# Kernel tuning notes

Measured on AMD Instinct MI355X. Metric: run time of the kernel, lower is better.

Reference implementation:

```python
import jax, jax.numpy as jnp
import numpy as np

T = 4096          # total packed tokens
SEG = 512         # segment length (position_ids reset every SEG)
D = 768           # hidden_size
H = 12            # num_attention_heads
DH = D // H       # head_dim = 64
THETA = 160000.0  # global_rope_theta (layer_id=0 -> global attention)


def setup_inputs() -> dict:
    key = jax.random.key(0)
    k1, k2, k3 = jax.random.split(key, 3)
    hidden_states = jax.random.normal(k1, (T, D), dtype=jnp.float32)
    # torch Linear weights stored transposed: here [in, out] for x @ W
    Wqkv = jax.random.normal(k2, (D, 3 * D), dtype=jnp.float32) / np.sqrt(D).astype(np.float32)
    Wo = jax.random.normal(k3, (D, D), dtype=jnp.float32) / np.sqrt(D).astype(np.float32)
    # packed batch: 8 segments of length SEG, position ids restart at 0
    position_ids = (jnp.arange(T, dtype=jnp.int32) % SEG)
    return {"hidden_states": hidden_states, "Wqkv": Wqkv, "Wo": Wo,
            "position_ids": position_ids}


def _neox_rope(x, pos):
    # x: [T, H, DH]; neox-style rotary over full head_dim
    half = DH // 2
    inv_freq = 1.0 / (THETA ** (jnp.arange(half, dtype=jnp.float32) * 2.0 / DH))
    freqs = pos.astype(jnp.float32)[:, None] * inv_freq[None, :]   # [T, half]
    cos = jnp.cos(freqs)[:, None, :]                               # [T, 1, half]
    sin = jnp.sin(freqs)[:, None, :]
    x1, x2 = x[..., :half], x[..., half:]
    return jnp.concatenate([x1 * cos - x2 * sin, x2 * cos + x1 * sin], axis=-1)


def reference(hidden_states, Wqkv, Wo, position_ids):
    qkv = hidden_states @ Wqkv                         # [T, 3D]
    q, k, v = jnp.split(qkv, 3, axis=-1)
    q = q.reshape(T, H, DH)
    k = k.reshape(T, H, DH)
    v = v.reshape(T, H, DH)
    q = _neox_rope(q, position_ids)
    k = _neox_rope(k, position_ids)
    # segment id per token (position_ids==0 marks a new sequence)
    seg = jnp.cumsum((position_ids == 0).astype(jnp.int32)) - 1
    mask = seg[:, None] == seg[None, :]                # block-diagonal [T, T]
    scale = 1.0 / np.sqrt(DH).astype(np.float32)
    scores = jnp.einsum('thd,shd->hts', q, k) * scale  # [H, T, T]
    scores = jnp.where(mask[None, :, :], scores, jnp.float32(-1e30))
    attn = jax.nn.softmax(scores, axis=-1)
    out = jnp.einsum('hts,shd->thd', attn, v).reshape(T, D)
    return out @ Wo
```

## Files before the change

kernel.cpp:

```cpp
#include <hip/hip_runtime.h>
#include <hip/hip_bf16.h>
#include <math.h>

#define T_TOK 4096
#define D_MODEL 768
#define H_HEADS 12
#define DH 64
#define SEG 512
#define NSEG 8
#define QKV_LD 2304

typedef __bf16 bf16x8_t __attribute__((ext_vector_type(8)));
typedef float f32x4_t __attribute__((ext_vector_type(4)));
typedef float f32x16_t __attribute__((ext_vector_type(16)));

#define GBK 64
#define QSCALE 0.18033688011112042f

#define FENCED_BARRIER()                         \
    do {                                         \
        __builtin_amdgcn_sched_barrier(0);       \
        __builtin_amdgcn_s_barrier();            \
        __builtin_amdgcn_sched_barrier(0);       \
    } while (0)

__device__ __forceinline__ void tconv_body(const float* __restrict__ in,
                                           __hip_bfloat16* __restrict__ out,
                                           int N, int K, int bx, int by, int tid,
                                           float (*tile)[65]) {
    const int k0 = by * 64;
    const int n0 = bx * 64;
    const int rr = tid >> 4;
    const int cc = (tid & 15) * 4;
#pragma unroll
    for (int i = 0; i < 4; ++i) {
        int r = i * 16 + rr;
        float4 v = *(const float4*)(in + (size_t)(k0 + r) * N + n0 + cc);
        tile[r][cc] = v.x; tile[r][cc + 1] = v.y; tile[r][cc + 2] = v.z; tile[r][cc + 3] = v.w;
    }
    __syncthreads();
#pragma unroll
    for (int i = 0; i < 4; ++i) {
        int n = i * 16 + rr;
        union { __hip_bfloat16 h[4]; ushort4 u; } o;
        o.h[0] = __float2bfloat16(tile[cc + 0][n]);
        o.h[1] = __float2bfloat16(tile[cc + 1][n]);
        o.h[2] = __float2bfloat16(tile[cc + 2][n]);
        o.h[3] = __float2bfloat16(tile[cc + 3][n]);
        *(ushort4*)(out + (size_t)(n0 + n) * K + k0 + cc) = o.u;
    }
}

__global__ __launch_bounds__(256) void prep_inputs(const float* __restrict__ hidden,
                                                   const float* __restrict__ Wqkv,
                                                   const float* __restrict__ Wo,
                                                   const int* __restrict__ pos_ids,
                                                   __hip_bfloat16* __restrict__ Xb,
                                                   __hip_bfloat16* __restrict__ Wqkvt,
                                                   __hip_bfloat16* __restrict__ Wot,
                                                   float2* __restrict__ rtab) {
    __shared__ float tile[64][65];
    const int b = blockIdx.x;
    const int tid = threadIdx.x;
    if (b < 3072) {
        int i = b * 256 + tid;
        float4 v = ((const float4*)hidden)[i];
        union { __hip_bfloat16 h[4]; ushort4 u; } o;
        o.h[0] = __float2bfloat16(v.x); o.h[1] = __float2bfloat16(v.y);
        o.h[2] = __float2bfloat16(v.z); o.h[3] = __float2bfloat16(v.w);
        ((ushort4*)Xb)[i] = o.u;
    } else if (b < 3504) {
        int lb = b - 3072;
        tconv_body(Wqkv, Wqkvt, QKV_LD, D_MODEL, lb % 36, lb / 36, tid, tile);
    } else if (b < 3648) {
        int lb = b - 3504;
        tconv_body(Wo, Wot, D_MODEL, D_MODEL, lb % 12, lb / 12, tid, tile);
    } else {
        int idx = (b - 3648) * 256 + tid;
        int t = idx >> 5;
        int i = idx & 31;
        float pos = (float)pos_ids[t];
        float inv_freq = powf(160000.0f, -(float)i / 32.0f);
        float s, c;
        sincosf(pos * inv_freq, &s, &c);
        rtab[idx] = make_float2(c, s);
    }
}

__global__ __launch_bounds__(256) void gemm_qkv_fused(const __hip_bfloat16* __restrict__ A,
                                                      const __hip_bfloat16* __restrict__ Bt,
                                                      const float2* __restrict__ rtab,
                                                      __hip_bfloat16* __restrict__ Qb,
                                                      __hip_bfloat16* __restrict__ Kb,
                                                      __hip_bfloat16* __restrict__ Vtb) {
    __shared__ __hip_bfloat16 As[2][64 * GBK];
    __shared__ __hip_bfloat16 Bs[2][128 * GBK];
    const int tid = threadIdx.x;
    const int lane = tid & 63;
    const int wid = tid >> 6;
    const int wr = wid >> 1;
    const int wc = wid & 1;
    const int orig = blockIdx.y * 18 + blockIdx.x;
    const int wg = (orig & 7) * 144 + (orig >> 3);
    const int m0 = (wg / 18) * 64;
    const int n0 = (wg % 18) * 128;
    const int K = D_MODEL;

    f32x4_t acc[2][4];
#pragma unroll
    for (int i = 0; i < 2; ++i)
#pragma unroll
        for (int j = 0; j < 4; ++j) acc[i][j] = (f32x4_t){0.f, 0.f, 0.f, 0.f};

    const int lr = lane >> 3;
    const int gc = lane & 7;
    const int swzc = (gc ^ lr) << 3;
    const int fr = lane & 15;
    const int l4 = lane >> 4;
    const int fsw = fr & 7;

#define STAGE_Q(buf_, k0_)                                                            \
    do {                                                                              \
        _Pragma("unroll")                                                             \
        for (int i_ = 0; i_ < 2; ++i_) {                                              \
            const int row_ = wid * 16 + i_ * 8;                                       \
            const __hip_bfloat16* ga_ = A + (size_t)(m0 + row_ + lr) * K + (k0_) + swzc; \
            __builtin_amdgcn_global_load_lds(                                         \
                (const __attribute__((address_space(1))) void*)ga_,                   \
                (__attribute__((address_space(3))) void*)(As[buf_] + row_ * GBK), 16, 0, 0); \
        }                                                                             \
        _Pragma("unroll")                                                             \
        for (int i_ = 0; i_ < 4; ++i_) {                                              \
            const int row_ = wid * 32 + i_ * 8;                                       \
            const __hip_bfloat16* gb_ = Bt + (size_t)(n0 + row_ + lr) * K + (k0_) + swzc; \
            __builtin_amdgcn_global_load_lds(                                         \
                (const __attribute__((address_space(1))) void*)gb_,                   \
                (__attribute__((address_space(3))) void*)(Bs[buf_] + row_ * GBK), 16, 0, 0); \
        }                                                                             \
    } while (0)

    const int NKT = K / GBK;
    STAGE_Q(0, 0);
    for (int kt = 0; kt < NKT; ++kt) {
        const int cur = kt & 1;
        if (kt < NKT - 1) {
            STAGE_Q(cur ^ 1, (kt + 1) * GBK);
            asm volatile("s_waitcnt vmcnt(6)" ::: "memory");
        } else {
            asm volatile("s_waitcnt vmcnt(0)" ::: "memory");
        }
        FENCED_BARRIER();
#pragma unroll
        for (int kk = 0; kk < 2; ++kk) {
            const int rg = ((kk * 4 + l4) ^ fsw) << 3;
            bf16x8_t af[2], bfr[4];
#pragma unroll
            for (int mi = 0; mi < 2; ++mi)
                af[mi] = *(const bf16x8_t*)(As[cur] + (wr * 32 + mi * 16 + fr) * GBK + rg);
#pragma unroll
            for (int ni = 0; ni < 4; ++ni)
                bfr[ni] = *(const bf16x8_t*)(Bs[cur] + (wc * 64 + ni * 16 + fr) * GBK + rg);
#pragma unroll
            for (int mi = 0; mi < 2; ++mi)
#pragma unroll
                for (int ni = 0; ni < 4; ++ni)
                    acc[mi][ni] = __builtin_amdgcn_mfma_f32_16x16x32_bf16(
                        af[mi], bfr[ni], acc[mi][ni], 0, 0, 0);
        }
        asm volatile("" ::: "memory");
        FENCED_BARRIER();
    }
#undef STAGE_Q

    const int colbase = n0 + wc * 64;
    const int chunk = colbase >> 6;
    const int part = chunk / H_HEADS;
    const int h = chunk % H_HEADS;
    const int trow0 = m0 + wr * 32;

    if (part == 2) {
        const int seg = trow0 >> 9;
        const int key0 = (trow0 & 511) + l4 * 4;
        __hip_bfloat16* vdst = Vtb + ((size_t)(h * NSEG + seg) * DH) * SEG;
#pragma unroll
        for (int mi = 0; mi < 2; ++mi)
#pragma unroll
            for (int ni = 0; ni < 4; ++ni) {
                int d = ni * 16 + fr;
                union { __hip_bfloat16 h2[4]; ushort4 u; } o;
#pragma unroll
                for (int j = 0; j < 4; ++j) o.h2[j] = __float2bfloat16(acc[mi][ni][j]);
                *(ushort4*)(vdst + (size_t)d * SEG + key0 + mi * 16) = o.u;
            }
    } else {
        __hip_bfloat16* dst = (part == 0) ? Qb : Kb;
        const float scale = (part == 0) ? QSCALE : 1.0f;
#pragma unroll
        for (int mi = 0; mi < 2; ++mi)
#pragma unroll
            for (int j = 0; j < 4; ++j) {
                int t = trow0 + mi * 16 + l4 * 4 + j;
                const float2* tb = rtab + (size_t)t * 32;
                float2 cs0 = tb[fr];
                float2 cs1 = tb[16 + fr];
                __hip_bfloat16* op = dst + ((size_t)h * T_TOK + t) * DH;
                float x1, x2;
                x1 = acc[mi][0][j]; x2 = acc[mi][2][j];
                op[fr]      = __float2bfloat16((x1 * cs0.x - x2 * cs0.y) * scale);
                op[fr + 32] = __float2bfloat16((x2 * cs0.x + x1 * cs0.y) * scale);
                x1 = acc[mi][1][j]; x2 = acc[mi][3][j];
                op[16 + fr] = __float2bfloat16((x1 * cs1.x - x2 * cs1.y) * scale);
                op[48 + fr] = __float2bfloat16((x2 * cs1.x + x1 * cs1.y) * scale);
            }
    }
}

__global__ __launch_bounds__(256) void gemm_wo64(const __hip_bfloat16* __restrict__ A,
                                                 const __hip_bfloat16* __restrict__ Bt,
                                                 float* __restrict__ C) {
    __shared__ __hip_bfloat16 As[2][64 * GBK];
    __shared__ __hip_bfloat16 Bs[2][64 * GBK];
    const int tid = threadIdx.x;
    const int lane = tid & 63;
    const int wid = tid >> 6;
    const int wr = wid >> 1, wc = wid & 1;
    const int orig = blockIdx.y * 12 + blockIdx.x;
    const int wg = (orig & 7) * 96 + (orig >> 3);
    const int m0 = (wg / 12) * 64;
    const int n0 = (wg % 12) * 64;
    const int K = D_MODEL;
    const int N = D_MODEL;

    f32x4_t acc[2][2];
#pragma unroll
    for (int i = 0; i < 2; ++i)
#pragma unroll
        for (int j = 0; j < 2; ++j) acc[i][j] = (f32x4_t){0.f, 0.f, 0.f, 0.f};

    const int lr = lane >> 3;
    const int gc = lane & 7;
    const int swzc = (gc ^ lr) << 3;
    const int fr = lane & 15;
    const int l4 = lane >> 4;
    const int fsw = fr & 7;

#define STAGE_W(buf_, k0_)                                                            \
    do {                                                                              \
        _Pragma("unroll")                                                             \
        for (int i_ = 0; i_ < 2; ++i_) {                                              \
            const int row_ = i_ * 32 + wid * 8;                                       \
            const __hip_bfloat16* ga_ = A + (size_t)(m0 + row_ + lr) * K + (k0_) + swzc; \
            __builtin_amdgcn_global_load_lds(                                         \
                (const __attribute__((address_space(1))) void*)ga_,                   \
                (__attribute__((address_space(3))) void*)(As[buf_] + row_ * GBK), 16, 0, 0); \
            const __hip_bfloat16* gb_ = Bt + (size_t)(n0 + row_ + lr) * K + (k0_) + swzc; \
            __builtin_amdgcn_global_load_lds(                                         \
                (const __attribute__((address_space(1))) void*)gb_,                   \
                (__attribute__((address_space(3))) void*)(Bs[buf_] + row_ * GBK), 16, 0, 0); \
        }                                                                             \
    } while (0)

    const int NKT = K / GBK;
    STAGE_W(0, 0);
    for (int kt = 0; kt < NKT; ++kt) {
        const int cur = kt & 1;
        if (kt < NKT - 1) {
            STAGE_W(cur ^ 1, (kt + 1) * GBK);
            asm volatile("s_waitcnt vmcnt(4)" ::: "memory");
        } else {
            asm volatile("s_waitcnt vmcnt(0)" ::: "memory");
        }
        FENCED_BARRIER();
#pragma unroll
        for (int kk = 0; kk < 2; ++kk) {
            const int rg = ((kk * 4 + l4) ^ fsw) << 3;
            bf16x8_t af[2], bfr[2];
#pragma unroll
            for (int mi = 0; mi < 2; ++mi)
                af[mi] = *(const bf16x8_t*)(As[cur] + (wr * 32 + mi * 16 + fr) * GBK + rg);
#pragma unroll
            for (int ni = 0; ni < 2; ++ni)
                bfr[ni] = *(const bf16x8_t*)(Bs[cur] + (wc * 32 + ni * 16 + fr) * GBK + rg);
#pragma unroll
            for (int mi = 0; mi < 2; ++mi)
#pragma unroll
                for (int ni = 0; ni < 2; ++ni)
                    acc[mi][ni] = __builtin_amdgcn_mfma_f32_16x16x32_bf16(
                        af[mi], bfr[ni], acc[mi][ni], 0, 0, 0);
        }
        asm volatile("" ::: "memory");
        FENCED_BARRIER();
    }
#undef STAGE_W

    float* Cb = C + (size_t)(m0 + wr * 32) * N + n0 + wc * 32;
#pragma unroll
    for (int mi = 0; mi < 2; ++mi)
#pragma unroll
        for (int ni = 0; ni < 2; ++ni)
#pragma unroll
            for (int j = 0; j < 4; ++j) {
                int r = mi * 16 + (lane >> 4) * 4 + j;
                Cb[(size_t)r * N + ni * 16 + fr] = acc[mi][ni][j];
            }
}

__device__ __forceinline__ unsigned pk2(float a, float b) {
    unsigned ua = (unsigned)__bfloat16_as_ushort(__float2bfloat16(a));
    unsigned ub = (unsigned)__bfloat16_as_ushort(__float2bfloat16(b));
    return ua | (ub << 16);
}

__global__ __launch_bounds__(128) void attn_mfma(const __hip_bfloat16* __restrict__ Qb,
                                                 const __hip_bfloat16* __restrict__ Kb,
                                                 const __hip_bfloat16* __restrict__ Vtb,
                                                 __hip_bfloat16* __restrict__ attnb) {
    __shared__ __hip_bfloat16 KS[2][64 * 64];
    __shared__ __hip_bfloat16 VS[2][64 * 64];

    const int tid = threadIdx.x;
    const int lane = tid & 63;
    const int w = tid >> 6;
    const int hi = lane >> 5;
    const int l31 = lane & 31;
    const int orig = blockIdx.x;
    const int wg = (orig & 7) * 96 + (orig >> 3);
    const int qt = wg & 7;
    const int hs = wg >> 3;
    const int h = hs % H_HEADS;
    const int seg = hs / H_HEADS;
    const int t0 = seg * SEG + qt * 64 + w * 32;

    const __hip_bfloat16* kb = Kb + ((size_t)h * T_TOK + seg * SEG) * DH;
    const __hip_bfloat16* vb = Vtb + (size_t)(h * NSEG + seg) * DH * SEG;

    bf16x8_t qf[4];
    {
        const __hip_bfloat16* qp = Qb + ((size_t)h * T_TOK + t0 + l31) * DH + hi * 8;
#pragma unroll
        for (int s = 0; s < 4; ++s) qf[s] = *(const bf16x8_t*)(qp + s * 16);
    }

    const int gr = lane >> 3;
    const int gc = lane & 7;

#pragma unroll
    for (int i = 0; i < 4; ++i) {
        int G = i * 128 + w * 64;
        int rk = (G >> 3) + gr;
        const __hip_bfloat16* sk = kb + (size_t)rk * DH + ((gc ^ (rk & 7)) << 3);
        __builtin_amdgcn_global_load_lds(
            (const __attribute__((address_space(1))) void*)sk,
            (__attribute__((address_space(3))) void*)(&KS[0][G * 8]), 16, 0, 0);
        const __hip_bfloat16* sv = vb + (size_t)rk * SEG + ((gc ^ (rk & 7)) << 3);
        __builtin_amdgcn_global_load_lds(
            (const __attribute__((address_space(1))) void*)sv,
            (__attribute__((address_space(3))) void*)(&VS[0][G * 8]), 16, 0, 0);
    }
    __syncthreads();

    f32x16_t ot[2];
#pragma unroll
    for (int n = 0; n < 2; ++n)
#pragma unroll
        for (int r = 0; r < 16; ++r) ot[n][r] = 0.f;
    float lrun = 0.f;

    for (int kv = 0; kv < 8; ++kv) {
        const int bb = kv & 1;
        if (kv < 7) {
#pragma unroll
            for (int i = 0; i < 4; ++i) {
                int G = i * 128 + w * 64;
                int rk = (G >> 3) + gr;
                const __hip_bfloat16* sk = kb + (size_t)((kv + 1) * 64 + rk) * DH + ((gc ^ (rk & 7)) << 3);
                __builtin_amdgcn_global_load_lds(
                    (const __attribute__((address_space(1))) void*)sk,
                    (__attribute__((address_space(3))) void*)(&KS[bb ^ 1][G * 8]), 16, 0, 0);
                const __hip_bfloat16* sv = vb + (size_t)rk * SEG + (kv + 1) * 64 + ((gc ^ (rk & 7)) << 3);
                __builtin_amdgcn_global_load_lds(
                    (const __attribute__((address_space(1))) void*)sv,
                    (__attribute__((address_space(3))) void*)(&VS[bb ^ 1][G * 8]), 16, 0, 0);
            }
        }

        f32x16_t st[2];
#pragma unroll
        for (int t = 0; t < 2; ++t)
#pragma unroll
            for (int r = 0; r < 16; ++r) st[t][r] = 0.f;
#pragma unroll
        for (int s = 0; s < 4; ++s) {
            int gk = s * 2 + hi;
            bf16x8_t k0 = *(const bf16x8_t*)(&KS[bb][l31 * 64 + ((gk ^ (l31 & 7)) << 3)]);
            bf16x8_t k1 = *(const bf16x8_t*)(&KS[bb][(32 + l31) * 64 + ((gk ^ (l31 & 7)) << 3)]);
            st[0] = __builtin_amdgcn_mfma_f32_32x32x16_bf16(k0, qf[s], st[0], 0, 0, 0);
            st[1] = __builtin_amdgcn_mfma_f32_32x32x16_bf16(k1, qf[s], st[1], 0, 0, 0);
        }

        float psum = 0.f;
#pragma unroll
        for (int t = 0; t < 2; ++t)
#pragma unroll
            for (int r = 0; r < 16; ++r) {
                float p = exp2f(st[t][r]);
                st[t][r] = p;
                psum += p;
            }
        psum += __shfl_xor(psum, 32);
        lrun += psum;

        bf16x8_t pf[4];
#pragma unroll
        for (int t = 0; t < 2; ++t) {
            unsigned wv[8], ov[8];
#pragma unroll
            for (int j = 0; j < 8; ++j) wv[j] = pk2(st[t][2 * j], st[t][2 * j + 1]);
#pragma unroll
            for (int j = 0; j < 8; ++j) ov[j] = (unsigned)__shfl_xor((int)wv[j], 32);
#pragma unroll
            for (int sh = 0; sh < 2; ++sh) {
                int b = sh * 4;
                union { unsigned u[4]; bf16x8_t v; } u8;
                u8.u[0] = hi ? ov[b + 2] : wv[b + 0];
                u8.u[1] = hi ? ov[b + 3] : wv[b + 1];
                u8.u[2] = hi ? wv[b + 2] : ov[b + 0];
                u8.u[3] = hi ? wv[b + 3] : ov[b + 1];
                pf[t * 2 + sh] = u8.v;
            }
        }

#pragma unroll
        for (int s = 0; s < 4; ++s) {
            int gk = s * 2 + hi;
            bf16x8_t v0 = *(const bf16x8_t*)(&VS[bb][l31 * 64 + ((gk ^ (l31 & 7)) << 3)]);
            bf16x8_t v1 = *(const bf16x8_t*)(&VS[bb][(32 + l31) * 64 + ((gk ^ (l31 & 7)) << 3)]);
            ot[0] = __builtin_amdgcn_mfma_f32_32x32x16_bf16(v0, pf[s], ot[0], 0, 0, 0);
            ot[1] = __builtin_amdgcn_mfma_f32_32x32x16_bf16(v1, pf[s], ot[1], 0, 0, 0);
        }
        __syncthreads();
    }

    float invl = 1.0f / lrun;
    ushort* Os = (ushort*)&KS[0][0];
    const int wbase = w * (64 * 33);
#pragma unroll
    for (int n = 0; n < 2; ++n)
#pragma unroll
        for (int r = 0; r < 16; ++r) {
            int d = n * 32 + (r & 3) + 8 * (r >> 2) + 4 * hi;
            Os[wbase + d * 33 + l31] = __bfloat16_as_ushort(__float2bfloat16(ot[n][r] * invl));
        }
    __syncthreads();
    {
        unsigned ow2[16];
#pragma unroll
        for (int j = 0; j < 16; ++j) {
            unsigned lo = Os[wbase + (hi * 32 + 2 * j) * 33 + l31];
            unsigned hh = Os[wbase + (hi * 32 + 2 * j + 1) * 33 + l31];
            ow2[j] = lo | (hh << 16);
        }
        uint4* gd = (uint4*)(attnb + (size_t)(t0 + l31) * D_MODEL + h * DH + hi * 32);
        gd[0] = make_uint4(ow2[0], ow2[1], ow2[2], ow2[3]);
        gd[1] = make_uint4(ow2[4], ow2[5], ow2[6], ow2[7]);
        gd[2] = make_uint4(ow2[8], ow2[9], ow2[10], ow2[11]);
        gd[3] = make_uint4(ow2[12], ow2[13], ow2[14], ow2[15]);
    }
}

extern "C" void kernel_launch(void* const* d_in, const int* in_sizes, int n_in,
                              void* d_out, int out_size, void* d_ws, size_t ws_size,
                              hipStream_t stream) {
    const float* hidden = (const float*)d_in[0];
    const float* Wqkv   = (const float*)d_in[1];
    const float* Wo     = (const float*)d_in[2];
    const int*   pos    = (const int*)d_in[3];

    char* ws = (char*)d_ws;
    __hip_bfloat16* Xb    = (__hip_bfloat16*)(ws);
    __hip_bfloat16* Wqkvt = (__hip_bfloat16*)(ws + 6291456);
    __hip_bfloat16* Wot   = (__hip_bfloat16*)(ws + 9830400);
    __hip_bfloat16* Qb    = (__hip_bfloat16*)(ws + 11010048);
    __hip_bfloat16* Kb    = (__hip_bfloat16*)(ws + 17301504);
    __hip_bfloat16* Vtb   = (__hip_bfloat16*)(ws + 23592960);
    __hip_bfloat16* attnb = (__hip_bfloat16*)(ws + 29884416);
    float2* rtab          = (float2*)(ws + 36175872);
    float* out = (float*)d_out;

    prep_inputs<<<4160, 256, 0, stream>>>(hidden, Wqkv, Wo, pos, Xb, Wqkvt, Wot, rtab);

    gemm_qkv_fused<<<dim3(18, T_TOK / 64), 256, 0, stream>>>(
        Xb, Wqkvt, rtab, Qb, Kb, Vtb);

    attn_mfma<<<768, 128, 0, stream>>>(Qb, Kb, Vtb, attnb);

    gemm_wo64<<<dim3(D_MODEL / 64, T_TOK / 64), 256, 0, stream>>>(
        attnb, Wot, out);
}
```

Measured before the change: 70.82 us.

## Split KV tiles across two wave pairs in attention and reduce partial outputs

The attention kernel now runs 256 threads per block. Two wave pairs each handle alternating KV tiles (split-K over the segment), each loading its own tile into a separate LDS buffer. The double-buffered prefetch pipeline is replaced by a load, wait and barrier on every iteration. At the end, one pair writes its partial O and row sums to LDS and the other pair adds them before normalizing and storing. This doubles the waves per block to raise parallelism and latency hiding, at the cost of losing load/compute overlap within a wave and adding an LDS reduction step. Skipping the max subtraction in softmax stays correct only because the scores are summed unnormalized across both halves.

```diff
diff --git a/kernel.cpp b/kernel.cpp
--- a/kernel.cpp
+++ b/kernel.cpp
@@ -311,7 +311,7 @@
     return ua | (ub << 16);
 }
 
-__global__ __launch_bounds__(128) void attn_mfma(const __hip_bfloat16* __restrict__ Qb,
+__global__ __launch_bounds__(256) void attn_mfma(const __hip_bfloat16* __restrict__ Qb,
                                                  const __hip_bfloat16* __restrict__ Kb,
                                                  const __hip_bfloat16* __restrict__ Vtb,
                                                  __hip_bfloat16* __restrict__ attnb) {
@@ -321,6 +321,8 @@
     const int tid = threadIdx.x;
     const int lane = tid & 63;
     const int w = tid >> 6;
+    const int qw = w & 1;
+    const int par = w >> 1;
     const int hi = lane >> 5;
     const int l31 = lane & 31;
     const int orig = blockIdx.x;
@@ -329,7 +331,7 @@
     const int hs = wg >> 3;
     const int h = hs % H_HEADS;
     const int seg = hs / H_HEADS;
-    const int t0 = seg * SEG + qt * 64 + w * 32;
+    const int t0 = seg * SEG + qt * 64 + qw * 32;
 
     const __hip_bfloat16* kb = Kb + ((size_t)h * T_TOK + seg * SEG) * DH;
     const __hip_bfloat16* vb = Vtb + (size_t)(h * NSEG + seg) * DH * SEG;
@@ -344,21 +346,6 @@
     const int gr = lane >> 3;
     const int gc = lane & 7;
 
-#pragma unroll
-    for (int i = 0; i < 4; ++i) {
-        int G = i * 128 + w * 64;
-        int rk = (G >> 3) + gr;
-        const __hip_bfloat16* sk = kb + (size_t)rk * DH + ((gc ^ (rk & 7)) << 3);
-        __builtin_amdgcn_global_load_lds(
-            (const __attribute__((address_space(1))) void*)sk,
-            (__attribute__((address_space(3))) void*)(&KS[0][G * 8]), 16, 0, 0);
-        const __hip_bfloat16* sv = vb + (size_t)rk * SEG + ((gc ^ (rk & 7)) << 3);
-        __builtin_amdgcn_global_load_lds(
-            (const __attribute__((address_space(1))) void*)sv,
-            (__attribute__((address_space(3))) void*)(&VS[0][G * 8]), 16, 0, 0);
-    }
-    __syncthreads();
-
     f32x16_t ot[2];
 #pragma unroll
     for (int n = 0; n < 2; ++n)
@@ -366,23 +353,23 @@
         for (int r = 0; r < 16; ++r) ot[n][r] = 0.f;
     float lrun = 0.f;
 
-    for (int kv = 0; kv < 8; ++kv) {
-        const int bb = kv & 1;
-        if (kv < 7) {
-#pragma unroll
-            for (int i = 0; i < 4; ++i) {
-                int G = i * 128 + w * 64;
-                int rk = (G >> 3) + gr;
-                const __hip_bfloat16* sk = kb + (size_t)((kv + 1) * 64 + rk) * DH + ((gc ^ (rk & 7)) << 3);
-                __builtin_amdgcn_global_load_lds(
-                    (const __attribute__((address_space(1))) void*)sk,
-                    (__attribute__((address_space(3))) void*)(&KS[bb ^ 1][G * 8]), 16, 0, 0);
-                const __hip_bfloat16* sv = vb + (size_t)rk * SEG + (kv + 1) * 64 + ((gc ^ (rk & 7)) << 3);
-                __builtin_amdgcn_global_load_lds(
-                    (const __attribute__((address_space(1))) void*)sv,
-                    (__attribute__((address_space(3))) void*)(&VS[bb ^ 1][G * 8]), 16, 0, 0);
-            }
-        }
+    for (int it = 0; it < 4; ++it) {
+        const int tile = 2 * it + par;
+#pragma unroll
+        for (int i = 0; i < 4; ++i) {
+            int G = i * 128 + qw * 64;
+            int rk = (G >> 3) + gr;
+            const __hip_bfloat16* sk = kb + (size_t)(tile * 64 + rk) * DH + ((gc ^ (rk & 7)) << 3);
+            __builtin_amdgcn_global_load_lds(
+                (const __attribute__((address_space(1))) void*)sk,
+                (__attribute__((address_space(3))) void*)(&KS[par][G * 8]), 16, 0, 0);
+            const __hip_bfloat16* sv = vb + (size_t)rk * SEG + tile * 64 + ((gc ^ (rk & 7)) << 3);
+            __builtin_amdgcn_global_load_lds(
+                (const __attribute__((address_space(1))) void*)sv,
+                (__attribute__((address_space(3))) void*)(&VS[par][G * 8]), 16, 0, 0);
+        }
+        asm volatile("s_waitcnt vmcnt(0)" ::: "memory");
+        FENCED_BARRIER();
 
         f32x16_t st[2];
 #pragma unroll
@@ -392,8 +379,8 @@
 #pragma unroll
         for (int s = 0; s < 4; ++s) {
             int gk = s * 2 + hi;
-            bf16x8_t k0 = *(const bf16x8_t*)(&KS[bb][l31 * 64 + ((gk ^ (l31 & 7)) << 3)]);
-            bf16x8_t k1 = *(const bf16x8_t*)(&KS[bb][(32 + l31) * 64 + ((gk ^ (l31 & 7)) << 3)]);
+            bf16x8_t k0 = *(const bf16x8_t*)(&KS[par][l31 * 64 + ((gk ^ (l31 & 7)) << 3)]);
+            bf16x8_t k1 = *(const bf16x8_t*)(&KS[par][(32 + l31) * 64 + ((gk ^ (l31 & 7)) << 3)]);
             st[0] = __builtin_amdgcn_mfma_f32_32x32x16_bf16(k0, qf[s], st[0], 0, 0, 0);
             st[1] = __builtin_amdgcn_mfma_f32_32x32x16_bf16(k1, qf[s], st[1], 0, 0, 0);
         }
@@ -433,31 +420,48 @@
 #pragma unroll
         for (int s = 0; s < 4; ++s) {
             int gk = s * 2 + hi;
-            bf16x8_t v0 = *(const bf16x8_t*)(&VS[bb][l31 * 64 + ((gk ^ (l31 & 7)) << 3)]);
-            bf16x8_t v1 = *(const bf16x8_t*)(&VS[bb][(32 + l31) * 64 + ((gk ^ (l31 & 7)) << 3)]);
+            bf16x8_t v0 = *(const bf16x8_t*)(&VS[par][l31 * 64 + ((gk ^ (l31 & 7)) << 3)]);
+            bf16x8_t v1 = *(const bf16x8_t*)(&VS[par][(32 + l31) * 64 + ((gk ^ (l31 & 7)) << 3)]);
             ot[0] = __builtin_amdgcn_mfma_f32_32x32x16_bf16(v0, pf[s], ot[0], 0, 0, 0);
             ot[1] = __builtin_amdgcn_mfma_f32_32x32x16_bf16(v1, pf[s], ot[1], 0, 0, 0);
         }
-        __syncthreads();
-    }
+        FENCED_BARRIER();
+    }
+
+    float* redO = (float*)KS;
+    float* redL = (float*)VS;
+    if (par == 1) {
+#pragma unroll
+        for (int n = 0; n < 2; ++n)
+#pragma unroll
+            for (int r = 0; r < 16; ++r)
+                redO[(qw * 32 + n * 16 + r) * 64 + lane] = ot[n][r];
+        redL[qw * 64 + lane] = lrun;
+    }
+    FENCED_BARRIER();
+    if (par == 1) return;
+#pragma unroll
+    for (int n = 0; n < 2; ++n)
+#pragma unroll
+        for (int r = 0; r < 16; ++r)
+            ot[n][r] += redO[(qw * 32 + n * 16 + r) * 64 + lane];
+    lrun += redL[qw * 64 + lane];
 
     float invl = 1.0f / lrun;
-    ushort* Os = (ushort*)&KS[0][0];
-    const int wbase = w * (64 * 33);
+    ushort* Os = (ushort*)VS + 256 + qw * 2112;
 #pragma unroll
     for (int n = 0; n < 2; ++n)
 #pragma unroll
         for (int r = 0; r < 16; ++r) {
             int d = n * 32 + (r & 3) + 8 * (r >> 2) + 4 * hi;
-            Os[wbase + d * 33 + l31] = __bfloat16_as_ushort(__float2bfloat16(ot[n][r] * invl));
-        }
-    __syncthreads();
+            Os[d * 33 + l31] = __bfloat16_as_ushort(__float2bfloat16(ot[n][r] * invl));
+        }
     {
         unsigned ow2[16];
 #pragma unroll
         for (int j = 0; j < 16; ++j) {
-            unsigned lo = Os[wbase + (hi * 32 + 2 * j) * 33 + l31];
-            unsigned hh = Os[wbase + (hi * 32 + 2 * j + 1) * 33 + l31];
+            unsigned lo = Os[(hi * 32 + 2 * j) * 33 + l31];
+            unsigned hh = Os[(hi * 32 + 2 * j + 1) * 33 + l31];
             ow2[j] = lo | (hh << 16);
         }
         uint4* gd = (uint4*)(attnb + (size_t)(t0 + l31) * D_MODEL + h * DH + hi * 32);
@@ -492,7 +496,7 @@
     gemm_qkv_fused<<<dim3(18, T_TOK / 64), 256, 0, stream>>>(
         Xb, Wqkvt, rtab, Qb, Kb, Vtb);
 
-    attn_mfma<<<768, 128, 0, stream>>>(Qb, Kb, Vtb, attnb);
+    attn_mfma<<<768, 256, 0, stream>>>(Qb, Kb, Vtb, attnb);
 
     gemm_wo64<<<dim3(D_MODEL / 64, T_TOK / 64), 256, 0, stream>>>(
         attnb, Wot, out);
```

Result: faster. 65.87 us, median of 3 (-7.0%).
